# Optimization experiments

Measured on AMD Instinct MI355X. Metric: run time of the kernel, lower is better.

The kernel has to match this reference:

```python
import jax, jax.numpy as jnp
import numpy as np
from jax import lax

NUM_QUBITS = 4
NUM_LAYERS = 2
EPS = 1e-5  # BatchNorm eps; eval mode with running_mean=0, running_var=1


def _cnot_ring_matrix():
    # CNOT(0,1); CNOT(1,2); CNOT(2,3); CNOT(3,0) as one 16x16 permutation.
    # PennyLane convention: wire 0 is the most-significant bit of the basis index.
    M = np.zeros((16, 16), dtype=np.complex64)
    for b in range(16):
        bb = b
        for cw, tw in [(0, 1), (1, 2), (2, 3), (3, 0)]:
            if (bb >> (3 - cw)) & 1:
                bb ^= 1 << (3 - tw)
        M[bb, b] = 1.0
    return M

CNOT_RING = jnp.asarray(_cnot_ring_matrix())
# ZSIGNS[w, b] = <b|Z_w|b> = +/-1
ZSIGNS = jnp.asarray(np.array([[1.0 - 2.0 * ((b >> (3 - w)) & 1) for b in range(16)]
                               for w in range(NUM_QUBITS)], dtype=np.float32))


def conv_bn_relu(x, w, b, gamma, beta):
    # Conv2d(k=3, pad=1) + BatchNorm2d (eval: mean=0, var=1) + ReLU, NCHW
    x = lax.conv_general_dilated(x, w, (1, 1), ((1, 1), (1, 1)),
                                 dimension_numbers=('NCHW', 'OIHW', 'NCHW'))
    x = x + b[None, :, None, None]
    x = gamma[None, :, None, None] * x * (1.0 / np.sqrt(1.0 + EPS)) + beta[None, :, None, None]
    return jax.nn.relu(x)


def maxpool2(x):
    return lax.reduce_window(x, -jnp.inf, lax.max, (1, 1, 2, 2), (1, 1, 2, 2), 'VALID')


def avgpool2(x):
    return lax.reduce_window(x, 0.0, lax.add, (1, 1, 2, 2), (1, 1, 2, 2), 'VALID') * 0.25


def quantum_layer(x, weights):
    # x: [B, 16] softmax outputs. Amplitude-encode (abs + L2 normalize), then
    # BasicEntanglerLayers (RX rotations + CNOT ring) x NUM_LAYERS, then <Z_i>.
    psi = jnp.abs(x)
    psi = psi / jnp.linalg.norm(psi, axis=1, keepdims=True)
    psi = psi.astype(jnp.complex64)  # [B, 16] batched statevectors
    for l in range(NUM_LAYERS):
        c = jnp.cos(weights[l] * 0.5).astype(jnp.complex64)
        s = jnp.sin(weights[l] * 0.5).astype(jnp.complex64)
        U = jnp.ones((1, 1), dtype=jnp.complex64)
        for q in range(NUM_QUBITS):
            g = jnp.stack([jnp.stack([c[q], -1j * s[q]]),
                           jnp.stack([-1j * s[q], c[q]])])  # RX(theta_q)
            U = jnp.kron(U, g)
        U = CNOT_RING @ U  # rotations first, then entangling ring
        psi = psi @ U.T    # batched apply: [B,16] x [16,16]
    probs = jnp.real(psi * jnp.conj(psi))  # [B, 16]
    return probs @ ZSIGNS.T                # [B, 4] Pauli-Z expvals


def setup_inputs() -> dict:
    key = jax.random.key(0)
    ks = jax.random.split(key, 16)
    B = 1024
    f32 = jnp.float32

    def w(k, shape, fan_in):
        return jax.random.normal(k, shape, dtype=f32) * np.float32(1.0 / np.sqrt(fan_in))

    inp = {
        'x': jax.random.normal(ks[0], (B, 3, 32, 32), dtype=f32),
        'conv1_w': w(ks[1], (32, 3, 3, 3), 3 * 9), 'conv1_b': jnp.zeros((32,), f32),
        'bn1_g': jnp.ones((32,), f32), 'bn1_b': jnp.zeros((32,), f32),
        'conv2_w': w(ks[2], (64, 32, 3, 3), 32 * 9), 'conv2_b': jnp.zeros((64,), f32),
        'bn2_g': jnp.ones((64,), f32), 'bn2_b': jnp.zeros((64,), f32),
        'conv3_w': w(ks[3], (128, 64, 3, 3), 64 * 9), 'conv3_b': jnp.zeros((128,), f32),
        'bn3_g': jnp.ones((128,), f32), 'bn3_b': jnp.zeros((128,), f32),
        'fr1_w': w(ks[4], (512, 2048), 2048), 'fr1_b': jnp.zeros((512,), f32),
        'fr2_w': w(ks[5], (16, 512), 512), 'fr2_b': jnp.zeros((16,), f32),
        'q_weights': jax.random.uniform(ks[6], (NUM_LAYERS, NUM_QUBITS), dtype=f32,
                                        minval=0.0, maxval=2.0 * np.pi),
        'h1_w': w(ks[7], (128, 4), 4), 'h1_b': jnp.zeros((128,), f32),
        'bnh_g': jnp.ones((128,), f32), 'bnh_b': jnp.zeros((128,), f32),
        'h2_w': w(ks[8], (100, 128), 128), 'h2_b': jnp.zeros((100,), f32),
    }
    return inp


def reference(x, conv1_w, conv1_b, bn1_g, bn1_b, conv2_w, conv2_b, bn2_g, bn2_b,
              conv3_w, conv3_b, bn3_g, bn3_b, fr1_w, fr1_b, fr2_w, fr2_b,
              q_weights, h1_w, h1_b, bnh_g, bnh_b, h2_w, h2_b):
    # classical_net (CIFAR100 branch)
    h = conv_bn_relu(x, conv1_w, conv1_b, bn1_g, bn1_b)
    h = maxpool2(h)                                   # [B,32,16,16]
    h = conv_bn_relu(h, conv2_w, conv2_b, bn2_g, bn2_b)
    h = maxpool2(h)                                   # [B,64,8,8]
    h = conv_bn_relu(h, conv3_w, conv3_b, bn3_g, bn3_b)  # [B,128,8,8]
    h = avgpool2(h)                                   # AdaptiveAvgPool2d((4,4)): 8->4
    h = h.reshape(h.shape[0], -1)                     # [B, 2048]
    # feature_reducer
    h = jax.nn.relu(h @ fr1_w.T + fr1_b)
    f = jax.nn.softmax(h @ fr2_w.T + fr2_b, axis=1)   # [B, 16]
    # quantum layer (batched 4-qubit statevector sim)
    q = quantum_layer(f, q_weights)                   # [B, 4]
    # head (BN eval-mode, Dropout inactive)
    y = q @ h1_w.T + h1_b
    y = bnh_g * y * (1.0 / np.sqrt(1.0 + EPS)) + bnh_b
    y = jax.nn.relu(y)
    return y @ h2_w.T + h2_b                          # [B, 100]
```

## Files before the change

### kernel.cpp

```cpp
#include <hip/hip_runtime.h>
#include <math.h>

#define NB 1024
static constexpr float BN_INV = 0.99999500003749975f;

typedef __attribute__((ext_vector_type(8))) short short8;
typedef __attribute__((ext_vector_type(4))) float f32x4;

__device__ inline short f2bf(float f) {
  union { float f; unsigned u; } v;
  v.f = f;
  unsigned u = v.u;
  u += 0x7fff + ((u >> 16) & 1);
  return (short)(u >> 16);
}

__global__ void k_prepack(const float* __restrict__ c2w, const float* __restrict__ c2b,
                          const float* __restrict__ g2, const float* __restrict__ be2,
                          const float* __restrict__ c3w, const float* __restrict__ c3b,
                          const float* __restrict__ g3, const float* __restrict__ be3,
                          short* __restrict__ wp2, short* __restrict__ wp3,
                          float* __restrict__ scsh) {
  int i = blockIdx.x * 256 + threadIdx.x;
  int stride = gridDim.x * 256;
  for (int e = i; e < 18432; e += stride) {
    int j = e & 7, lane = (e >> 3) & 63, ct = (e >> 9) & 3, off = e >> 11;
    int co = ct * 16 + (lane & 15), ci = (lane >> 4) * 8 + j;
    wp2[e] = f2bf(c2w[(co * 32 + ci) * 9 + off]);
  }
  for (int e = i; e < 73728; e += stride) {
    int j = e & 7, lane = (e >> 3) & 63, ct = (e >> 9) & 7, oh = e >> 12;
    int half = oh & 1, off = oh >> 1;
    int co = ct * 16 + (lane & 15), ci = half * 32 + (lane >> 4) * 8 + j;
    wp3[e] = f2bf(c3w[(co * 64 + ci) * 9 + off]);
  }
  if (i < 64) {
    float sc = g2[i] * BN_INV;
    scsh[i] = sc;
    scsh[64 + i] = sc * c2b[i] + be2[i];
  } else if (i < 192) {
    int c = i - 64;
    float sc = g3[c] * BN_INV;
    scsh[128 + c] = sc;
    scsh[256 + c] = sc * c3b[c] + be3[c];
  }
}

__global__ __launch_bounds__(256) void k_convfused(
    const float* __restrict__ x, const float* __restrict__ w1,
    const float* __restrict__ b1, const float* __restrict__ g1,
    const float* __restrict__ be1, const short* __restrict__ wp2,
    const short* __restrict__ wp3, const float* __restrict__ scsh,
    const float* __restrict__ fr1w, short* __restrict__ wfr1,
    short* __restrict__ out3 ) {
  __shared__ __align__(16) char smem[40320];
  const int tid = threadIdx.x;
  const int bx = blockIdx.x;

  if (bx >= NB) {
    int i = (bx - NB) * 256 + tid;
    for (int e = i; e < 524288; e += 128 * 256) {
      float2 f = ((const float2*)fr1w)[e];
      unsigned lo = (unsigned)(unsigned short)f2bf(f.x);
      unsigned hi = (unsigned)(unsigned short)f2bf(f.y);
      ((unsigned*)wfr1)[e] = (hi << 16) | lo;
    }
    return;
  }

  short* inT = (short*)smem;
  float* tile = (float*)(smem + 25920);
  short* inT3 = (short*)(smem + 25920);

  const int b = bx;

  const float* xb = x + b * 3 * 32 * 32;
  for (int i = tid; i < 6480; i += 256) ((int*)inT)[i] = 0;
  for (int i = tid; i < 3 * 34 * 34; i += 256) {
    int c = i / 1156;
    int rem = i - c * 1156;
    int r = rem / 34;
    int col = rem - r * 34;
    int iy = r - 1, ix = col - 1;
    float v = 0.f;
    if (iy >= 0 && iy < 32 && ix >= 0 && ix < 32)
      v = xb[(c * 32 + iy) * 32 + ix];
    tile[i] = v;
  }
  __syncthreads();

  {
    const int tx = tid & 15, ty = tid >> 4;
    float win[3][4][4];
#pragma unroll
    for (int c = 0; c < 3; ++c)
#pragma unroll
      for (int r = 0; r < 4; ++r)
#pragma unroll
        for (int cc = 0; cc < 4; ++cc)
          win[c][r][cc] = tile[c * 1156 + (2 * ty + r) * 34 + 2 * tx + cc];

    short cv[32];
#pragma unroll
    for (int co = 0; co < 32; ++co) {
      const float* wp = w1 + co * 27;
      float a00 = 0.f, a01 = 0.f, a10 = 0.f, a11 = 0.f;
#pragma unroll
      for (int c = 0; c < 3; ++c)
#pragma unroll
        for (int ky = 0; ky < 3; ++ky)
#pragma unroll
          for (int kx = 0; kx < 3; ++kx) {
            float wv = wp[c * 9 + ky * 3 + kx];
            a00 = fmaf(win[c][ky][kx], wv, a00);
            a01 = fmaf(win[c][ky][kx + 1], wv, a01);
            a10 = fmaf(win[c][ky + 1][kx], wv, a10);
            a11 = fmaf(win[c][ky + 1][kx + 1], wv, a11);
          }
      float gg = g1[co] * BN_INV, bt = be1[co], bs = b1[co];
      float v0 = fmaxf(fmaf(gg, a00 + bs, bt), 0.f);
      float v1 = fmaxf(fmaf(gg, a01 + bs, bt), 0.f);
      float v2 = fmaxf(fmaf(gg, a10 + bs, bt), 0.f);
      float v3 = fmaxf(fmaf(gg, a11 + bs, bt), 0.f);
      cv[co] = f2bf(fmaxf(fmaxf(v0, v1), fmaxf(v2, v3)));
    }
    short8* dst = (short8*)&inT[((ty + 1) * 18 + (tx + 1)) * 40];
#pragma unroll
    for (int k = 0; k < 4; ++k) {
      short8 v;
#pragma unroll
      for (int j = 0; j < 8; ++j) v[j] = cv[k * 8 + j];
      dst[k] = v;
    }
  }
  __syncthreads();

  for (int i = tid; i < 3600; i += 256) ((int*)inT3)[i] = 0;
  __syncthreads();

  const int wid = tid >> 6, lane = tid & 63, q = lane >> 4, n = lane & 15;

  {
    const short8* wv = (const short8*)wp2;
    f32x4 acc[4][4];
#pragma unroll
    for (int t = 0; t < 4; ++t)
#pragma unroll
      for (int ct = 0; ct < 4; ++ct) acc[t][ct] = (f32x4)0.f;

#pragma unroll
    for (int off = 0; off < 9; ++off) {
      const int ky = off / 3, kx = off % 3;
      short8 a[4];
#pragma unroll
      for (int ct = 0; ct < 4; ++ct) a[ct] = wv[(off * 4 + ct) * 64 + lane];
#pragma unroll
      for (int t = 0; t < 4; ++t) {
        int y = 4 * wid + t;
        short8 bf = *(const short8*)&inT[((y + ky) * 18 + (n + kx)) * 40 + q * 8];
#pragma unroll
        for (int ct = 0; ct < 4; ++ct)
          acc[t][ct] = __builtin_amdgcn_mfma_f32_16x16x32_bf16(a[ct], bf,
                                                               acc[t][ct], 0, 0, 0);
      }
    }

    const float* sc2 = scsh;
    const float* sh2 = scsh + 64;
#pragma unroll
    for (int ct = 0; ct < 4; ++ct) {
      float vm[4][4];
#pragma unroll
      for (int t = 0; t < 4; ++t)
#pragma unroll
        for (int r = 0; r < 4; ++r) {
          int co = ct * 16 + q * 4 + r;
          float v = fmaf(sc2[co], acc[t][ct][r], sh2[co]);
          v = fmaxf(v, 0.f);
          vm[t][r] = fmaxf(v, __shfl_xor(v, 1));
        }
#pragma unroll
      for (int pp = 0; pp < 2; ++pp)
#pragma unroll
        for (int r = 0; r < 4; ++r) {
          float m = fmaxf(vm[2 * pp][r], vm[2 * pp + 1][r]);
          if ((n & 1) == 0) {
            int co = ct * 16 + q * 4 + r;
            int y2 = 2 * wid + pp, x2 = n >> 1;
            inT3[((y2 + 1) * 10 + (x2 + 1)) * 72 + co] = f2bf(m);
          }
        }
    }
  }
  __syncthreads();

  {
    const short8* wv = (const short8*)wp3;
    f32x4 acc[4][2];
#pragma unroll
    for (int c = 0; c < 4; ++c)
#pragma unroll
      for (int tt = 0; tt < 2; ++tt) acc[c][tt] = (f32x4)0.f;

    const int ct0 = (wid >> 1) * 4;
    const int t0 = (wid & 1) * 2;
#pragma unroll
    for (int off = 0; off < 9; ++off) {
      const int ky = off / 3, kx = off % 3;
#pragma unroll
      for (int half = 0; half < 2; ++half) {
        short8 a[4];
#pragma unroll
        for (int c = 0; c < 4; ++c)
          a[c] = wv[((off * 2 + half) * 8 + ct0 + c) * 64 + lane];
#pragma unroll
        for (int tt = 0; tt < 2; ++tt) {
          int y = 2 * (t0 + tt) + (n >> 3), xx = n & 7;
          short8 bf = *(const short8*)&inT3[((y + ky) * 10 + (xx + kx)) * 72 +
                                            half * 32 + q * 8];
#pragma unroll
          for (int c = 0; c < 4; ++c)
            acc[c][tt] = __builtin_amdgcn_mfma_f32_16x16x32_bf16(a[c], bf,
                                                                 acc[c][tt], 0, 0, 0);
        }
      }
    }

    const float* sc3 = scsh + 128;
    const float* sh3 = scsh + 256;
#pragma unroll
    for (int c = 0; c < 4; ++c) {
      int ct = ct0 + c;
#pragma unroll
      for (int tt = 0; tt < 2; ++tt) {
        int t = t0 + tt;
#pragma unroll
        for (int r = 0; r < 4; ++r) {
          int co = ct * 16 + q * 4 + r;
          float v = fmaf(sc3[co], acc[c][tt][r], sh3[co]);
          v = fmaxf(v, 0.f);
          float s = v + __shfl_xor(v, 1);
          s += __shfl_xor(s, 8);
          if ((n & 9) == 0)
            out3[(size_t)b * 2048 + co * 16 + t * 4 + (n >> 1)] = f2bf(s * 0.25f);
        }
      }
    }
  }
}

__global__ __launch_bounds__(256) void k_fr1m(
    const short* __restrict__ A, const short* __restrict__ W,
    const float* __restrict__ bias, float* __restrict__ C) {
  __shared__ __align__(16) short As[32 * 72];
  __shared__ __align__(16) short Bs[32 * 72];
  const int m0 = blockIdx.x * 32;
  const int n0 = blockIdx.y * 32;
  const int tid = threadIdx.x;
  const int w = tid >> 6, lane = tid & 63, q = lane >> 4, n = lane & 15;
  const int mt = w >> 1, nt = w & 1;
  const int srow = tid >> 3, sc = tid & 7;

  f32x4 acc = (f32x4)0.f;
  const short* Ab = A + (size_t)(m0 + srow) * 2048 + sc * 8;
  const short* Wb = W + (size_t)(n0 + srow) * 2048 + sc * 8;

  for (int k0 = 0; k0 < 2048; k0 += 64) {
    short8 av = *(const short8*)(Ab + k0);
    short8 bv = *(const short8*)(Wb + k0);
    __syncthreads();
    *(short8*)&As[srow * 72 + sc * 8] = av;
    *(short8*)&Bs[srow * 72 + sc * 8] = bv;
    __syncthreads();
#pragma unroll
    for (int kk = 0; kk < 2; ++kk) {
      short8 bfrag = *(const short8*)&Bs[(nt * 16 + n) * 72 + kk * 32 + q * 8];
      short8 afrag = *(const short8*)&As[(mt * 16 + n) * 72 + kk * 32 + q * 8];
      acc = __builtin_amdgcn_mfma_f32_16x16x32_bf16(afrag, bfrag, acc, 0, 0, 0);
    }
  }
#pragma unroll
  for (int r = 0; r < 4; ++r) {
    int m = m0 + mt * 16 + q * 4 + r;
    int nn = n0 + nt * 16 + n;
    C[(size_t)m * 512 + nn] = fmaxf(acc[r] + bias[nn], 0.f);
  }
}

__global__ __launch_bounds__(64) void k_tail(
    const float* __restrict__ H, const float* __restrict__ W2,
    const float* __restrict__ b2, const float* __restrict__ qw,
    const float* __restrict__ h1w, const float* __restrict__ h1b,
    const float* __restrict__ bg, const float* __restrict__ bb,
    const float* __restrict__ h2w, const float* __restrict__ h2b,
    float* __restrict__ out) {
  __shared__ float hbuf[512];
  __shared__ float ybuf[128];
  const int b = blockIdx.x;
  const int lane = threadIdx.x;
  const float* hrow = H + b * 512;
  *(float4*)&hbuf[lane * 4] = *(const float4*)&hrow[lane * 4];
  *(float4*)&hbuf[256 + lane * 4] = *(const float4*)&hrow[256 + lane * 4];
  __syncthreads();

  const int j = lane & 15;
  const int grpk = lane >> 4;
  float partial = 0.f;
  const float* wrow = W2 + j * 512 + grpk * 128;
  const float* hb = hbuf + grpk * 128;
#pragma unroll
  for (int k = 0; k < 128; k += 4) {
    float4 wv = *(const float4*)&wrow[k];
    partial = fmaf(wv.x, hb[k + 0], partial);
    partial = fmaf(wv.y, hb[k + 1], partial);
    partial = fmaf(wv.z, hb[k + 2], partial);
    partial = fmaf(wv.w, hb[k + 3], partial);
  }
  partial += __shfl_xor(partial, 16);
  partial += __shfl_xor(partial, 32);
  float logit = partial + b2[j];

  float m = logit;
#pragma unroll
  for (int d = 1; d < 16; d <<= 1) m = fmaxf(m, __shfl_xor(m, d));
  float e = expf(logit - m);
  float s = e;
#pragma unroll
  for (int d = 1; d < 16; d <<= 1) s += __shfl_xor(s, d);
  float p = e / s;

  float n2 = p * p;
#pragma unroll
  for (int d = 1; d < 16; d <<= 1) n2 += __shfl_xor(n2, d);
  float amp = p / sqrtf(n2);
  float re = amp, im = 0.f;

#pragma unroll
  for (int l = 0; l < 2; ++l) {
#pragma unroll
    for (int q = 0; q < 4; ++q) {
      float th = qw[l * 4 + q] * 0.5f;
      float c = cosf(th), sn = sinf(th);
      int mask = 1 << (3 - q);
      float pre = __shfl_xor(re, mask);
      float pim = __shfl_xor(im, mask);
      float nre = fmaf(c, re, sn * pim);
      float nim = fmaf(c, im, -sn * pre);
      re = nre;
      im = nim;
    }
    int src = j;
    if (src & 1) src ^= 8;
    if (src & 2) src ^= 1;
    if (src & 4) src ^= 2;
    if (src & 8) src ^= 4;
    int srclane = (lane & 48) | src;
    re = __shfl(re, srclane);
    im = __shfl(im, srclane);
  }

  float prob = re * re + im * im;
  float qv[4];
#pragma unroll
  for (int w = 0; w < 4; ++w) {
    float sgn = ((j >> (3 - w)) & 1) ? -1.f : 1.f;
    float cwv = prob * sgn;
    cwv += __shfl_xor(cwv, 1);
    cwv += __shfl_xor(cwv, 2);
    cwv += __shfl_xor(cwv, 4);
    cwv += __shfl_xor(cwv, 8);
    qv[w] = cwv;
  }

#pragma unroll
  for (int t = 0; t < 2; ++t) {
    int jj = lane + 64 * t;
    float4 hw = *(const float4*)&h1w[jj * 4];
    float y = h1b[jj];
    y = fmaf(hw.x, qv[0], y);
    y = fmaf(hw.y, qv[1], y);
    y = fmaf(hw.z, qv[2], y);
    y = fmaf(hw.w, qv[3], y);
    y = fmaf(bg[jj] * BN_INV, y, bb[jj]);
    ybuf[jj] = fmaxf(y, 0.f);
  }
  __syncthreads();

#pragma unroll
  for (int t = 0; t < 2; ++t) {
    int k = lane + 64 * t;
    if (k < 100) {
      const float* wr = h2w + k * 128;
      float o = h2b[k];
#pragma unroll
      for (int jj = 0; jj < 128; jj += 4) {
        float4 wv = *(const float4*)&wr[jj];
        o = fmaf(wv.x, ybuf[jj + 0], o);
        o = fmaf(wv.y, ybuf[jj + 1], o);
        o = fmaf(wv.z, ybuf[jj + 2], o);
        o = fmaf(wv.w, ybuf[jj + 3], o);
      }
      out[b * 100 + k] = o;
    }
  }
}

extern "C" void kernel_launch(void* const* d_in, const int* in_sizes, int n_in,
                              void* d_out, int out_size, void* d_ws,
                              size_t ws_size, hipStream_t stream) {
  const float* x = (const float*)d_in[0];
  const float* c1w = (const float*)d_in[1];
  const float* c1b = (const float*)d_in[2];
  const float* g1 = (const float*)d_in[3];
  const float* be1 = (const float*)d_in[4];
  const float* c2w = (const float*)d_in[5];
  const float* c2b = (const float*)d_in[6];
  const float* g2 = (const float*)d_in[7];
  const float* be2 = (const float*)d_in[8];
  const float* c3w = (const float*)d_in[9];
  const float* c3b = (const float*)d_in[10];
  const float* g3 = (const float*)d_in[11];
  const float* be3 = (const float*)d_in[12];
  const float* fr1w = (const float*)d_in[13];
  const float* fr1b = (const float*)d_in[14];
  const float* fr2w = (const float*)d_in[15];
  const float* fr2b = (const float*)d_in[16];
  const float* qwts = (const float*)d_in[17];
  const float* h1w = (const float*)d_in[18];
  const float* h1b = (const float*)d_in[19];
  const float* bhg = (const float*)d_in[20];
  const float* bhb = (const float*)d_in[21];
  const float* h2w = (const float*)d_in[22];
  const float* h2b = (const float*)d_in[23];
  float* out = (float*)d_out;

  float* ws = (float*)d_ws;
  short* out3bf = (short*)ws;
  float* h1 = ws + 1048576;
  short* wfr1 = (short*)(ws + 1572864);
  short* wp2 = (short*)(ws + 2097152);
  short* wp3 = (short*)(ws + 2106368);
  float* scsh = ws + 2143232;

  k_prepack<<<96, 256, 0, stream>>>(c2w, c2b, g2, be2, c3w, c3b, g3, be3,
                                    wp2, wp3, scsh);
  k_convfused<<<NB + 128, 256, 0, stream>>>(x, c1w, c1b, g1, be1, wp2, wp3,
                                            scsh, fr1w, wfr1, out3bf);
  k_fr1m<<<dim3(32, 16), 256, 0, stream>>>(out3bf, wfr1, fr1b, h1);
  k_tail<<<NB, 64, 0, stream>>>(h1, fr2w, fr2b, qwts, h1w, h1b, bhg, bhb, h2w,
                                h2b, out);
}
```

Baseline: 207.2 us.

## Move conv1 to bf16 MFMA with prepacked BN-folded weights and vectorized input load

Conv1 moves off per-thread scalar FMA into 16x16x32 bf16 MFMA. Its weights are prepacked with the BN scale folded in, and the 3 input channels are zero-padded to 8 in a channel-interleaved bf16 smem tile. The input image is loaded with 16-byte vector loads instead of per-element index arithmetic, and the 2x2 maxpool is done with lane shuffles. This removes the heavy scalar FMA work and the repeated global weight reads in conv1, at the cost of wasted MFMA lanes on padded channels and reduced input precision (bf16 instead of fp32). Launch bounds also now ask for 4 blocks per CU.

```diff
diff --git a/kernel.cpp b/kernel.cpp
--- a/kernel.cpp
+++ b/kernel.cpp
@@ -5,6 +5,7 @@
 static constexpr float BN_INV = 0.99999500003749975f;
 
 typedef __attribute__((ext_vector_type(8))) short short8;
+typedef __attribute__((ext_vector_type(4))) short s16x4;
 typedef __attribute__((ext_vector_type(4))) float f32x4;
 
 __device__ inline short f2bf(float f) {
@@ -15,14 +16,23 @@
   return (short)(u >> 16);
 }
 
-__global__ void k_prepack(const float* __restrict__ c2w, const float* __restrict__ c2b,
+__global__ void k_prepack(const float* __restrict__ c1w, const float* __restrict__ c1b,
+                          const float* __restrict__ g1, const float* __restrict__ be1,
+                          const float* __restrict__ c2w, const float* __restrict__ c2b,
                           const float* __restrict__ g2, const float* __restrict__ be2,
                           const float* __restrict__ c3w, const float* __restrict__ c3b,
                           const float* __restrict__ g3, const float* __restrict__ be3,
-                          short* __restrict__ wp2, short* __restrict__ wp3,
-                          float* __restrict__ scsh) {
+                          short* __restrict__ wp1, short* __restrict__ wp2,
+                          short* __restrict__ wp3, float* __restrict__ scsh) {
   int i = blockIdx.x * 256 + threadIdx.x;
   int stride = gridDim.x * 256;
+  for (int e = i; e < 9216; e += stride) {
+    int j = e & 7, lane = (e >> 3) & 63, ct = (e >> 9) & 1, off = e >> 10;
+    int co = ct * 16 + (lane & 15), k = (lane >> 4) * 8 + j;
+    float v = 0.f;
+    if (k < 3) v = c1w[(co * 3 + k) * 9 + off] * g1[co] * BN_INV;
+    wp1[e] = f2bf(v);
+  }
   for (int e = i; e < 18432; e += stride) {
     int j = e & 7, lane = (e >> 3) & 63, ct = (e >> 9) & 3, off = e >> 11;
     int co = ct * 16 + (lane & 15), ci = (lane >> 4) * 8 + j;
@@ -43,16 +53,17 @@
     float sc = g3[c] * BN_INV;
     scsh[128 + c] = sc;
     scsh[256 + c] = sc * c3b[c] + be3[c];
-  }
-}
-
-__global__ __launch_bounds__(256) void k_convfused(
-    const float* __restrict__ x, const float* __restrict__ w1,
-    const float* __restrict__ b1, const float* __restrict__ g1,
-    const float* __restrict__ be1, const short* __restrict__ wp2,
-    const short* __restrict__ wp3, const float* __restrict__ scsh,
-    const float* __restrict__ fr1w, short* __restrict__ wfr1,
-    short* __restrict__ out3 ) {
+  } else if (i < 224) {
+    int c = i - 192;
+    scsh[384 + c] = g1[c] * BN_INV * c1b[c] + be1[c];
+  }
+}
+
+__global__ __launch_bounds__(256, 4) void k_convfused(
+    const float* __restrict__ x, const short* __restrict__ wp1,
+    const short* __restrict__ wp2, const short* __restrict__ wp3,
+    const float* __restrict__ scsh, const float* __restrict__ fr1w,
+    short* __restrict__ wfr1, short* __restrict__ out3 ) {
   __shared__ __align__(16) char smem[40320];
   const int tid = threadIdx.x;
   const int bx = blockIdx.x;
@@ -69,76 +80,86 @@
   }
 
   short* inT = (short*)smem;
-  float* tile = (float*)(smem + 25920);
+  short* tile1 = (short*)(smem + 25920);
   short* inT3 = (short*)(smem + 25920);
 
   const int b = bx;
-
-  const float* xb = x + b * 3 * 32 * 32;
+  const int wid = tid >> 6, lane = tid & 63, q = lane >> 4, n = lane & 15;
+
+  const float* xb = x + b * 3072;
+  f32x4 xf[3];
+#pragma unroll
+  for (int k = 0; k < 3; ++k) xf[k] = ((const f32x4*)xb)[tid + 256 * k];
   for (int i = tid; i < 6480; i += 256) ((int*)inT)[i] = 0;
-  for (int i = tid; i < 3 * 34 * 34; i += 256) {
-    int c = i / 1156;
-    int rem = i - c * 1156;
-    int r = rem / 34;
-    int col = rem - r * 34;
-    int iy = r - 1, ix = col - 1;
-    float v = 0.f;
-    if (iy >= 0 && iy < 32 && ix >= 0 && ix < 32)
-      v = xb[(c * 32 + iy) * 32 + ix];
-    tile[i] = v;
+  for (int i = tid; i < 2312; i += 256) ((int*)tile1)[i] = 0;
+  __syncthreads();
+#pragma unroll
+  for (int k = 0; k < 3; ++k) {
+    int e0 = (tid + 256 * k) * 4;
+#pragma unroll
+    for (int jj = 0; jj < 4; ++jj) {
+      int e = e0 + jj;
+      int c = e >> 10, rem = e & 1023, iy = rem >> 5, ix = rem & 31;
+      tile1[((iy + 1) * 34 + (ix + 1)) * 4 + c] = f2bf(xf[k][jj]);
+    }
   }
   __syncthreads();
 
   {
-    const int tx = tid & 15, ty = tid >> 4;
-    float win[3][4][4];
-#pragma unroll
-    for (int c = 0; c < 3; ++c)
-#pragma unroll
-      for (int r = 0; r < 4; ++r)
-#pragma unroll
-        for (int cc = 0; cc < 4; ++cc)
-          win[c][r][cc] = tile[c * 1156 + (2 * ty + r) * 34 + 2 * tx + cc];
-
-    short cv[32];
-#pragma unroll
-    for (int co = 0; co < 32; ++co) {
-      const float* wp = w1 + co * 27;
-      float a00 = 0.f, a01 = 0.f, a10 = 0.f, a11 = 0.f;
-#pragma unroll
-      for (int c = 0; c < 3; ++c)
-#pragma unroll
-        for (int ky = 0; ky < 3; ++ky)
-#pragma unroll
-          for (int kx = 0; kx < 3; ++kx) {
-            float wv = wp[c * 9 + ky * 3 + kx];
-            a00 = fmaf(win[c][ky][kx], wv, a00);
-            a01 = fmaf(win[c][ky][kx + 1], wv, a01);
-            a10 = fmaf(win[c][ky + 1][kx], wv, a10);
-            a11 = fmaf(win[c][ky + 1][kx + 1], wv, a11);
+    const short8* wv1 = (const short8*)wp1;
+    float sh1[2][4];
+#pragma unroll
+    for (int ct = 0; ct < 2; ++ct)
+#pragma unroll
+      for (int r = 0; r < 4; ++r) sh1[ct][r] = scsh[384 + ct * 16 + q * 4 + r];
+
+    const s16x4 z4 = (s16x4)0;
+#pragma unroll
+    for (int h = 0; h < 2; ++h) {
+      f32x4 acc[2][8];
+#pragma unroll
+      for (int ct = 0; ct < 2; ++ct)
+#pragma unroll
+        for (int yy = 0; yy < 8; ++yy) acc[ct][yy] = (f32x4)0.f;
+
+#pragma unroll
+      for (int off = 0; off < 9; ++off) {
+        const int kyy = off / 3, kxx = off % 3;
+        short8 a0 = wv1[(off * 2 + 0) * 64 + lane];
+        short8 a1 = wv1[(off * 2 + 1) * 64 + lane];
+#pragma unroll
+        for (int yy = 0; yy < 8; ++yy) {
+          int row = 8 * wid + yy + kyy;
+          s16x4 blo = *(const s16x4*)&tile1[(row * 34 + h * 16 + kxx + n) * 4];
+          short8 bfr = __builtin_shufflevector(blo, z4, 0, 1, 2, 3, 4, 5, 6, 7);
+          acc[0][yy] =
+              __builtin_amdgcn_mfma_f32_16x16x32_bf16(a0, bfr, acc[0][yy], 0, 0, 0);
+          acc[1][yy] =
+              __builtin_amdgcn_mfma_f32_16x16x32_bf16(a1, bfr, acc[1][yy], 0, 0, 0);
+        }
+      }
+#pragma unroll
+      for (int ct = 0; ct < 2; ++ct)
+#pragma unroll
+        for (int yp = 0; yp < 4; ++yp)
+#pragma unroll
+          for (int r = 0; r < 4; ++r) {
+            float v0 = fmaxf(acc[ct][2 * yp][r] + sh1[ct][r], 0.f);
+            float v1 = fmaxf(acc[ct][2 * yp + 1][r] + sh1[ct][r], 0.f);
+            float m = fmaxf(v0, v1);
+            m = fmaxf(m, __shfl_xor(m, 1));
+            if ((n & 1) == 0) {
+              int co = ct * 16 + q * 4 + r;
+              int yq = 4 * wid + yp, xq = 8 * h + (n >> 1);
+              inT[((yq + 1) * 18 + (xq + 1)) * 40 + co] = f2bf(m);
+            }
           }
-      float gg = g1[co] * BN_INV, bt = be1[co], bs = b1[co];
-      float v0 = fmaxf(fmaf(gg, a00 + bs, bt), 0.f);
-      float v1 = fmaxf(fmaf(gg, a01 + bs, bt), 0.f);
-      float v2 = fmaxf(fmaf(gg, a10 + bs, bt), 0.f);
-      float v3 = fmaxf(fmaf(gg, a11 + bs, bt), 0.f);
-      cv[co] = f2bf(fmaxf(fmaxf(v0, v1), fmaxf(v2, v3)));
-    }
-    short8* dst = (short8*)&inT[((ty + 1) * 18 + (tx + 1)) * 40];
-#pragma unroll
-    for (int k = 0; k < 4; ++k) {
-      short8 v;
-#pragma unroll
-      for (int j = 0; j < 8; ++j) v[j] = cv[k * 8 + j];
-      dst[k] = v;
     }
   }
   __syncthreads();
 
   for (int i = tid; i < 3600; i += 256) ((int*)inT3)[i] = 0;
   __syncthreads();
-
-  const int wid = tid >> 6, lane = tid & 63, q = lane >> 4, n = lane & 15;
 
   {
     const short8* wv = (const short8*)wp2;
@@ -441,11 +462,12 @@
   short* wp2 = (short*)(ws + 2097152);
   short* wp3 = (short*)(ws + 2106368);
   float* scsh = ws + 2143232;
-
-  k_prepack<<<96, 256, 0, stream>>>(c2w, c2b, g2, be2, c3w, c3b, g3, be3,
-                                    wp2, wp3, scsh);
-  k_convfused<<<NB + 128, 256, 0, stream>>>(x, c1w, c1b, g1, be1, wp2, wp3,
-                                            scsh, fr1w, wfr1, out3bf);
+  short* wp1 = (short*)(ws + 2143744);
+
+  k_prepack<<<96, 256, 0, stream>>>(c1w, c1b, g1, be1, c2w, c2b, g2, be2, c3w,
+                                    c3b, g3, be3, wp1, wp2, wp3, scsh);
+  k_convfused<<<NB + 128, 256, 0, stream>>>(x, wp1, wp2, wp3, scsh, fr1w, wfr1,
+                                            out3bf);
   k_fr1m<<<dim3(32, 16), 256, 0, stream>>>(out3bf, wfr1, fr1b, h1);
   k_tail<<<NB, 64, 0, stream>>>(h1, fr2w, fr2b, qwts, h1w, h1b, bhg, bhb, h2w,
                                 h2b, out);
```

Result: slower. 304.0 us (+46.7%).
